# Optimization experiments

Hardware: AMD Instinct MI355X
Metric: run time of the kernel (lower is better)

The kernel has to match this reference:

```python
import jax, jax.numpy as jnp
import numpy as np
import math

N_HEADS = 12  # from init_kwargs


def setup_inputs() -> dict:
    key = jax.random.key(0)
    ks = jax.random.split(key, 9)
    B, N, D = 32, 577, 768
    s = 1.0 / math.sqrt(D)
    return {
        "x": jax.random.normal(ks[0], (B, N, D), jnp.float32),
        "Wq": jax.random.normal(ks[1], (D, D), jnp.float32) * s,
        "bq": jax.random.normal(ks[2], (D,), jnp.float32) * 0.02,
        "Wk": jax.random.normal(ks[3], (D, D), jnp.float32) * s,
        "bk": jax.random.normal(ks[4], (D,), jnp.float32) * 0.02,
        "Wv": jax.random.normal(ks[5], (D, D), jnp.float32) * s,
        "bv": jax.random.normal(ks[6], (D,), jnp.float32) * 0.02,
        "Wo": jax.random.normal(ks[7], (D, D), jnp.float32) * s,
        "bo": jax.random.normal(ks[8], (D,), jnp.float32) * 0.02,
    }


def reference(x, Wq, bq, Wk, bk, Wv, bv, Wo, bo):
    B, N, D = x.shape
    H = N_HEADS
    Hd = D // H
    # project then split heads (intended semantics of the torch module)
    q = (x @ Wq.T + bq).reshape(B, N, H, Hd)
    k = (x @ Wk.T + bk).reshape(B, N, H, Hd)
    v = (x @ Wv.T + bv).reshape(B, N, H, Hd)
    # NOTE: faithful quirk - scale by sqrt(d_size), not sqrt(head_dim)
    scores = jnp.einsum('bqhd,bkhd->bhqk', q, k) / math.sqrt(D)  # [B,H,N,N]
    # faithful quirk: mask = triu(ones); positions where mask==0 (strictly
    # lower triangle, k < q) are filled with float32 min -> anti-causal mask
    allowed = jnp.triu(jnp.ones((N, N), dtype=bool))
    scores = jnp.where(allowed, scores, jnp.finfo(jnp.float32).min)
    att = jax.nn.softmax(scores, axis=3)  # dropout p=0.0 -> identity
    out = jnp.einsum('bhqk,bkhd->bqhd', att, v).reshape(B, N, D)
    return out @ Wo.T + bo
```

## Files before the change

### kernel.cpp

```cpp
#include <hip/hip_runtime.h>
#include <cstdint>
#include <cstddef>


typedef __bf16 bf16;
typedef __bf16 bf16x4 __attribute__((ext_vector_type(4)));
typedef __bf16 bf16x8 __attribute__((ext_vector_type(8)));
typedef float  f32x4  __attribute__((ext_vector_type(4)));

#define DEVI __device__ __forceinline__

constexpr int BATCH = 32;
constexpr int NSEQ  = 577;
constexpr int DMODEL= 768;
constexpr int NHEAD = 12;
constexpr int HD    = 64;
constexpr int M_ROWS = BATCH * NSEQ;
constexpr int M_PAD  = 145 * 128;
constexpr int N_PAD  = 640;
constexpr int QKV_N  = 3 * DMODEL;
constexpr float QSCALE = 0.036084391824351615f * 1.4426950408889634f;

DEVI void async_copy16(const void* g, void* l) {
  void* gg = (void*)(uintptr_t)g;
  __builtin_amdgcn_global_load_lds(
      (__attribute__((address_space(1))) void*)gg,
      (__attribute__((address_space(3))) void*)l,
      16, 0, 0);
}

DEVI f32x4 mfma16(bf16x8 a, bf16x8 b, f32x4 c) {
  return __builtin_amdgcn_mfma_f32_16x16x32_bf16(a, b, c, 0, 0, 0);
}

__global__ __launch_bounds__(256) void cast_kernel(
    const float* __restrict__ x,
    const float* __restrict__ wq, const float* __restrict__ wk,
    const float* __restrict__ wv, const float* __restrict__ wo,
    bf16* __restrict__ xb, bf16* __restrict__ wcat, bf16* __restrict__ wob)
{
  constexpr int XQ = (M_ROWS * DMODEL) / 4;
  constexpr int WQ = (DMODEL * DMODEL) / 4;
  int idx = blockIdx.x * 256 + threadIdx.x;
  const float4* src; bf16* dst; int off;
  if (idx < XQ) { src = (const float4*)x; dst = xb; off = idx; }
  else {
    int u = idx - XQ; int w = u / WQ; off = u - w * WQ;
    src = (const float4*)(w == 0 ? wq : w == 1 ? wk : w == 2 ? wv : wo);
    dst = (w < 3) ? (wcat + (size_t)w * DMODEL * DMODEL) : wob;
  }
  float4 v = src[off];
  bf16x4 o;
  o[0] = (bf16)v.x; o[1] = (bf16)v.y; o[2] = (bf16)v.z; o[3] = (bf16)v.w;
  *(bf16x4*)(dst + (size_t)off * 4) = o;
}

template <int MODE>
__global__ __launch_bounds__(256) void gemm_bt(
    const bf16* __restrict__ A, const bf16* __restrict__ Bw,
    const float* __restrict__ bias0, const float* __restrict__ bias1,
    const float* __restrict__ bias2,
    float* __restrict__ Cout,
    bf16* __restrict__ Qb, bf16* __restrict__ Kb, bf16* __restrict__ Vtb)
{
  __shared__ __align__(16) bf16 As[128 * 32];
  __shared__ __align__(16) bf16 Bs[128 * 32];
  const int t = threadIdx.x;
  const int w = t >> 6, lane = t & 63;
  const int g = lane >> 4, cl = lane & 15;
  const int wm = (w >> 1) * 64, wn = (w & 1) * 64;
  const int m0 = blockIdx.y * 128, n0 = blockIdx.x * 128;

  f32x4 acc[4][4] = {};

  const bf16* Ag = A  + (size_t)(m0 + (t >> 2)) * 768 + (t & 3) * 8;
  const bf16* Bg = Bw + (size_t)(n0 + (t >> 2)) * 768 + (t & 3) * 8;
  char* lA = (char*)As + w * 1024;
  char* lB = (char*)Bs + w * 1024;

  for (int kb = 0; kb < 768; kb += 32) {
    async_copy16(Ag + kb,                    lA);
    async_copy16(Ag + kb + (size_t)64 * 768, lA + 4096);
    async_copy16(Bg + kb,                    lB);
    async_copy16(Bg + kb + (size_t)64 * 768, lB + 4096);
    __syncthreads();
    bf16x8 af[4], bfr[4];
#pragma unroll
    for (int i = 0; i < 4; ++i)
      af[i] = *(const bf16x8*)(As + (wm + i * 16 + cl) * 32 + g * 8);
#pragma unroll
    for (int j = 0; j < 4; ++j)
      bfr[j] = *(const bf16x8*)(Bs + (wn + j * 16 + cl) * 32 + g * 8);
#pragma unroll
    for (int i = 0; i < 4; ++i)
#pragma unroll
      for (int j = 0; j < 4; ++j)
        acc[i][j] = mfma16(af[i], bfr[j], acc[i][j]);
    __syncthreads();
  }

  if constexpr (MODE == 0) {
#pragma unroll
    for (int j = 0; j < 4; ++j) {
      const int n = n0 + wn + j * 16 + cl;
      const int which = n >= 1536 ? 2 : (n >= 768 ? 1 : 0);
      const int rem = n - which * 768;
      const int h = rem >> 6, d = rem & 63;
      const float bias = (which == 0 ? bias0 : which == 1 ? bias1 : bias2)[rem];
#pragma unroll
      for (int i = 0; i < 4; ++i) {
#pragma unroll
        for (int r = 0; r < 4; ++r) {
          const unsigned m = (unsigned)(m0 + wm + i * 16 + g * 4 + r);
          if (m >= (unsigned)M_ROWS) continue;
          const unsigned bb = m / 577u;
          const unsigned nq = m - bb * 577u;
          const float fv = acc[i][j][r] + bias;
          if (which == 0)
            Qb[((size_t)(bb * NHEAD + h) * N_PAD + nq) * HD + d] = (bf16)(fv * QSCALE);
          else if (which == 1)
            Kb[((size_t)(bb * NHEAD + h) * N_PAD + nq) * HD + d] = (bf16)fv;
          else
            Vtb[((size_t)(bb * NHEAD + h) * HD + d) * N_PAD + nq] = (bf16)fv;
        }
      }
    }
  } else {
#pragma unroll
    for (int j = 0; j < 4; ++j) {
      const int n = n0 + wn + j * 16 + cl;
      const float bias = bias0[n];
#pragma unroll
      for (int i = 0; i < 4; ++i) {
#pragma unroll
        for (int r = 0; r < 4; ++r) {
          const unsigned m = (unsigned)(m0 + wm + i * 16 + g * 4 + r);
          if (m < (unsigned)M_ROWS)
            Cout[(size_t)m * 768 + n] = acc[i][j][r] + bias;
        }
      }
    }
  }
}

__global__ __launch_bounds__(256) void attn_kernel(
    const bf16* __restrict__ Qb, const bf16* __restrict__ Kb,
    const bf16* __restrict__ Vtb, bf16* __restrict__ Ao)
{
  __shared__ __align__(16) bf16 Qs[128 * 64];
  __shared__ __align__(16) bf16 Ks[2][64 * 64];
  __shared__ __align__(16) bf16 Vs[2][64 * 64];
  __shared__ __align__(16) bf16 Ps[4 * 32 * 64];

  const int t = threadIdx.x, w = t >> 6, lane = t & 63;
  const int g = lane >> 4, cl = lane & 15;
  const int qt = blockIdx.x;
  const int bh = blockIdx.y;
  const size_t kqbase = (size_t)bh * (N_PAD * HD);
  const size_t vbase  = (size_t)bh * (HD * N_PAD);

  const int srow = t >> 3;
  const int scol = ((t & 7) ^ (srow & 7)) * 8;

  const bf16* Qg = Qb  + kqbase + (size_t)(qt * 128 + srow) * HD + scol;
  const bf16* Kg = Kb  + kqbase + (size_t)srow * HD + scol;
  const bf16* Vg = Vtb + vbase  + (size_t)srow * N_PAD + scol;

  const int jb0 = 2 * qt, nit = 10 - jb0;

#pragma unroll
  for (int c = 0; c < 4; ++c)
    async_copy16(Qg + (size_t)c * 32 * HD, (char*)Qs + c * 4096 + w * 1024);
#pragma unroll
  for (int c = 0; c < 2; ++c) {
    async_copy16(Kg + (size_t)(jb0 * 64 + c * 32) * HD,  (char*)Ks[0] + c * 4096 + w * 1024);
    async_copy16(Vg + jb0 * 64 + (size_t)(c * 32) * N_PAD, (char*)Vs[0] + c * 4096 + w * 1024);
  }
  __syncthreads();

  f32x4 oacc[2][4] = {};
  f32x4 lsum[2] = {};
  bf16x8 onesf;
#pragma unroll
  for (int e = 0; e < 8; ++e) onesf[e] = (bf16)(cl == 0 ? 1.0f : 0.0f);

  bf16* pw = Ps + w * 2048;
  const int qw0 = qt * 128 + w * 32;

  for (int it = 0; it < nit; ++it) {
    const int jb = jb0 + it;
    const int buf = it & 1;
    if (it + 1 < nit) {
      const int jn = jb + 1, nb = buf ^ 1;
#pragma unroll
      for (int c = 0; c < 2; ++c) {
        async_copy16(Kg + (size_t)(jn * 64 + c * 32) * HD,   (char*)Ks[nb] + c * 4096 + w * 1024);
        async_copy16(Vg + jn * 64 + (size_t)(c * 32) * N_PAD, (char*)Vs[nb] + c * 4096 + w * 1024);
      }
    }

    f32x4 s[2][4] = {};
#pragma unroll
    for (int ks = 0; ks < 2; ++ks) {
      const int ch = ((ks * 4 + g) ^ (cl & 7)) * 8;
#pragma unroll
      for (int f = 0; f < 2; ++f) {
        bf16x8 aq = *(const bf16x8*)(Qs + (w * 32 + f * 16 + cl) * 64 + ch);
#pragma unroll
        for (int j = 0; j < 4; ++j) {
          bf16x8 bk = *(const bf16x8*)(Ks[buf] + (j * 16 + cl) * 64 + ch);
          s[f][j] = mfma16(aq, bk, s[f][j]);
        }
      }
    }

    float p[2][4][4];
    const bool need_mask = (jb * 64 < qw0 + 32) || (jb == 9);
    if (need_mask) {
#pragma unroll
      for (int f = 0; f < 2; ++f)
#pragma unroll
        for (int j = 0; j < 4; ++j) {
          const int kg = jb * 64 + j * 16 + cl;
#pragma unroll
          for (int r = 0; r < 4; ++r) {
            const bool ok = (kg >= qw0 + f * 16 + g * 4 + r) && (kg < NSEQ);
            p[f][j][r] = ok ? exp2f(s[f][j][r]) : 0.f;
          }
        }
    } else {
#pragma unroll
      for (int f = 0; f < 2; ++f)
#pragma unroll
        for (int j = 0; j < 4; ++j)
#pragma unroll
          for (int r = 0; r < 4; ++r)
            p[f][j][r] = exp2f(s[f][j][r]);
    }

#pragma unroll
    for (int f = 0; f < 2; ++f)
#pragma unroll
      for (int j = 0; j < 4; ++j)
#pragma unroll
        for (int r = 0; r < 4; ++r) {
          const int row = f * 16 + g * 4 + r;
          const int col = j * 16 + cl;
          pw[row * 64 + ((col >> 3) ^ (row & 7)) * 8 + (col & 7)] = (bf16)p[f][j][r];
        }

#pragma unroll
    for (int ks = 0; ks < 2; ++ks) {
      const int ch = ((ks * 4 + g) ^ (cl & 7)) * 8;
#pragma unroll
      for (int f = 0; f < 2; ++f) {
        bf16x8 ap = *(const bf16x8*)(pw + (f * 16 + cl) * 64 + ch);
#pragma unroll
        for (int j = 0; j < 4; ++j) {
          bf16x8 bv = *(const bf16x8*)(Vs[buf] + (j * 16 + cl) * 64 + ch);
          oacc[f][j] = mfma16(ap, bv, oacc[f][j]);
        }
        lsum[f] = mfma16(ap, onesf, lsum[f]);
      }
    }
    __syncthreads();
  }

  const int b_ = bh / NHEAD, h_ = bh - (bh / NHEAD) * NHEAD;
#pragma unroll
  for (int f = 0; f < 2; ++f)
#pragma unroll
    for (int r = 0; r < 4; ++r) {
      const int qg = qw0 + f * 16 + g * 4 + r;
      const float l = __shfl(lsum[f][r], lane & 48, 64);
      if (qg >= NSEQ) continue;
      const float inv = 1.f / l;
      const size_t row = ((size_t)b_ * NSEQ + qg) * DMODEL + h_ * HD;
#pragma unroll
      for (int j = 0; j < 4; ++j)
        Ao[row + j * 16 + cl] = (bf16)(oacc[f][j][r] * inv);
    }
}

extern "C" void kernel_launch(void* const* d_in, const int* in_sizes, int n_in,
                              void* d_out, int out_size, void* d_ws, size_t ws_size,
                              hipStream_t stream) {
  const float* x  = (const float*)d_in[0];
  const float* Wq = (const float*)d_in[1];
  const float* bq = (const float*)d_in[2];
  const float* Wk = (const float*)d_in[3];
  const float* bk = (const float*)d_in[4];
  const float* Wv = (const float*)d_in[5];
  const float* bv = (const float*)d_in[6];
  const float* Wo = (const float*)d_in[7];
  const float* bo = (const float*)d_in[8];

  char* ws = (char*)d_ws;
  size_t off = 0;
  auto alloc = [&](size_t bytes) -> char* {
    char* p = ws + off;
    off += (bytes + 255) & ~(size_t)255;
    return p;
  };
  bf16* xb   = (bf16*)alloc((size_t)M_PAD * DMODEL * 2);
  bf16* wcat = (bf16*)alloc((size_t)QKV_N * DMODEL * 2);
  bf16* wob  = (bf16*)alloc((size_t)DMODEL * DMODEL * 2);
  bf16* Qb   = (bf16*)alloc((size_t)BATCH * NHEAD * N_PAD * HD * 2);
  bf16* Kb   = (bf16*)alloc((size_t)BATCH * NHEAD * N_PAD * HD * 2);
  bf16* Vtb  = (bf16*)alloc((size_t)BATCH * NHEAD * HD * N_PAD * 2);
  bf16* Ao   = (bf16*)alloc((size_t)M_PAD * DMODEL * 2);
  (void)ws_size; (void)in_sizes; (void)n_in; (void)out_size;

  constexpr int XQ = (M_ROWS * DMODEL) / 4;
  constexpr int WQ = (DMODEL * DMODEL) / 4;
  const int cast_blocks = (XQ + 4 * WQ) / 256;
  cast_kernel<<<cast_blocks, 256, 0, stream>>>(x, Wq, Wk, Wv, Wo, xb, wcat, wob);

  gemm_bt<0><<<dim3(QKV_N / 128, M_PAD / 128), 256, 0, stream>>>(
      xb, wcat, bq, bk, bv, nullptr, Qb, Kb, Vtb);

  attn_kernel<<<dim3(5, BATCH * NHEAD), 256, 0, stream>>>(Qb, Kb, Vtb, Ao);

  gemm_bt<1><<<dim3(DMODEL / 128, M_PAD / 128), 256, 0, stream>>>(
      Ao, wob, bo, nullptr, nullptr, (float*)d_out, nullptr, nullptr, nullptr);
}
```

Baseline: 395.4 us.

## Swizzle GEMM LDS layout and move V transpose into separate kernel

The GEMM's shared-memory tile now uses an XOR swizzle on the 16-byte column chunk, applied both in the global-to-LDS copy and in the fragment reads, to reduce LDS bank conflicts. The QKV epilogue now writes V in the same row-major head layout as Q and K instead of scattering transposed stores. A new transpose_v kernel then builds the transposed V through shared memory with coalesced writes. This adds a kernel launch and an extra buffer round trip for V in exchange for coalesced stores and fewer bank conflicts.

```diff
diff --git a/kernel.cpp b/kernel.cpp
--- a/kernel.cpp
+++ b/kernel.cpp
@@ -61,7 +61,7 @@
     const float* __restrict__ bias0, const float* __restrict__ bias1,
     const float* __restrict__ bias2,
     float* __restrict__ Cout,
-    bf16* __restrict__ Qb, bf16* __restrict__ Kb, bf16* __restrict__ Vtb)
+    bf16* __restrict__ Qb, bf16* __restrict__ Kb, bf16* __restrict__ Vb)
 {
   __shared__ __align__(16) bf16 As[128 * 32];
   __shared__ __align__(16) bf16 Bs[128 * 32];
@@ -73,10 +73,13 @@
 
   f32x4 acc[4][4] = {};
 
-  const bf16* Ag = A  + (size_t)(m0 + (t >> 2)) * 768 + (t & 3) * 8;
-  const bf16* Bg = Bw + (size_t)(n0 + (t >> 2)) * 768 + (t & 3) * 8;
+  const int srow = t >> 2;
+  const int cg   = (t & 3) ^ ((t >> 3) & 3);
+  const bf16* Ag = A  + (size_t)(m0 + srow) * 768 + cg * 8;
+  const bf16* Bg = Bw + (size_t)(n0 + srow) * 768 + cg * 8;
   char* lA = (char*)As + w * 1024;
   char* lB = (char*)Bs + w * 1024;
+  const int ch = (g ^ ((cl >> 1) & 3)) * 8;
 
   for (int kb = 0; kb < 768; kb += 32) {
     async_copy16(Ag + kb,                    lA);
@@ -87,10 +90,10 @@
     bf16x8 af[4], bfr[4];
 #pragma unroll
     for (int i = 0; i < 4; ++i)
-      af[i] = *(const bf16x8*)(As + (wm + i * 16 + cl) * 32 + g * 8);
+      af[i] = *(const bf16x8*)(As + (wm + i * 16 + cl) * 32 + ch);
 #pragma unroll
     for (int j = 0; j < 4; ++j)
-      bfr[j] = *(const bf16x8*)(Bs + (wn + j * 16 + cl) * 32 + g * 8);
+      bfr[j] = *(const bf16x8*)(Bs + (wn + j * 16 + cl) * 32 + ch);
 #pragma unroll
     for (int i = 0; i < 4; ++i)
 #pragma unroll
@@ -107,6 +110,8 @@
       const int rem = n - which * 768;
       const int h = rem >> 6, d = rem & 63;
       const float bias = (which == 0 ? bias0 : which == 1 ? bias1 : bias2)[rem];
+      bf16* dst = which == 0 ? Qb : which == 1 ? Kb : Vb;
+      const float sc = which == 0 ? QSCALE : 1.0f;
 #pragma unroll
       for (int i = 0; i < 4; ++i) {
 #pragma unroll
@@ -115,13 +120,8 @@
           if (m >= (unsigned)M_ROWS) continue;
           const unsigned bb = m / 577u;
           const unsigned nq = m - bb * 577u;
-          const float fv = acc[i][j][r] + bias;
-          if (which == 0)
-            Qb[((size_t)(bb * NHEAD + h) * N_PAD + nq) * HD + d] = (bf16)(fv * QSCALE);
-          else if (which == 1)
-            Kb[((size_t)(bb * NHEAD + h) * N_PAD + nq) * HD + d] = (bf16)fv;
-          else
-            Vtb[((size_t)(bb * NHEAD + h) * HD + d) * N_PAD + nq] = (bf16)fv;
+          dst[((size_t)(bb * NHEAD + h) * N_PAD + nq) * HD + d] =
+              (bf16)((acc[i][j][r] + bias) * sc);
         }
       }
     }
@@ -141,6 +141,28 @@
       }
     }
   }
+}
+
+__global__ __launch_bounds__(256) void transpose_v(
+    const bf16* __restrict__ Vb, bf16* __restrict__ Vt)
+{
+  __shared__ __align__(16) bf16 Ls[64 * 72];
+  const int t = threadIdx.x;
+  const int bh = blockIdx.y, n0 = blockIdx.x * 64;
+
+  const bf16* src = Vb + ((size_t)bh * N_PAD + n0 + (t >> 3)) * HD + (t & 7) * 8;
+  *(bf16x8*)(Ls + (t >> 3) * 72 + (t & 7) * 8) = *(const bf16x8*)src;
+  *(bf16x8*)(Ls + ((t >> 3) + 32) * 72 + (t & 7) * 8) =
+      *(const bf16x8*)(src + (size_t)32 * HD);
+  __syncthreads();
+
+  const int d = t >> 2, nc = (t & 3) * 16;
+  bf16 o[16];
+#pragma unroll
+  for (int e = 0; e < 16; ++e) o[e] = Ls[(nc + e) * 72 + d];
+  bf16* dst = Vt + ((size_t)bh * HD + d) * N_PAD + n0 + nc;
+  *(bf16x8*)dst = *(bf16x8*)o;
+  *(bf16x8*)(dst + 8) = *(bf16x8*)(o + 8);
 }
 
 __global__ __launch_bounds__(256) void attn_kernel(
@@ -307,6 +329,7 @@
   bf16* wob  = (bf16*)alloc((size_t)DMODEL * DMODEL * 2);
   bf16* Qb   = (bf16*)alloc((size_t)BATCH * NHEAD * N_PAD * HD * 2);
   bf16* Kb   = (bf16*)alloc((size_t)BATCH * NHEAD * N_PAD * HD * 2);
+  bf16* Vb   = (bf16*)alloc((size_t)BATCH * NHEAD * N_PAD * HD * 2);
   bf16* Vtb  = (bf16*)alloc((size_t)BATCH * NHEAD * HD * N_PAD * 2);
   bf16* Ao   = (bf16*)alloc((size_t)M_PAD * DMODEL * 2);
   (void)ws_size; (void)in_sizes; (void)n_in; (void)out_size;
@@ -317,7 +340,9 @@
   cast_kernel<<<cast_blocks, 256, 0, stream>>>(x, Wq, Wk, Wv, Wo, xb, wcat, wob);
 
   gemm_bt<0><<<dim3(QKV_N / 128, M_PAD / 128), 256, 0, stream>>>(
-      xb, wcat, bq, bk, bv, nullptr, Qb, Kb, Vtb);
+      xb, wcat, bq, bk, bv, nullptr, Qb, Kb, Vb);
+
+  transpose_v<<<dim3(N_PAD / 64, BATCH * NHEAD), 256, 0, stream>>>(Vb, Vtb);
 
   attn_kernel<<<dim3(5, BATCH * NHEAD), 256, 0, stream>>>(Qb, Kb, Vtb, Ao);
 
```

Result: no change. 391.4 us (-1.0%).
